# Kernel optimization log

Hardware: AMD Instinct MI355X
Metric: run time of the kernel (lower is better)

The kernel has to match this reference:

```python
import jax, jax.numpy as jnp
import numpy as np

G, VPG, CPG, LPC = 32, 512, 1024, 3
N_VARS, N_CLAUSES = G * VPG, G * CPG
N_LITS = N_CLAUSES * LPC
FM, QM, ROUNDS = 128, 32, 4
EPS_NORM, EPS_LOG, EPS_SQRT = 1e-6, 1e-8, 1e-6


def _dense_init(key, fin, fout):
    w = jax.random.normal(key, (fin, fout), jnp.float32) * np.float32(np.sqrt(2.0 / (fin + fout)))
    return w, jnp.zeros((fout,), jnp.float32)


def setup_inputs():
    rng = np.random.default_rng(0)
    g_of_clause = np.repeat(np.arange(G), CPG)
    lit_clause = np.repeat(np.arange(N_CLAUSES), LPC).astype(np.int32)
    # each clause picks LPC variables from its own graph's variable block
    lit_var = (np.repeat(g_of_clause * VPG, LPC) + rng.integers(0, VPG, N_LITS)).astype(np.int32)
    lit_sign = (rng.integers(0, 2, N_LITS) * 2 - 1).astype(np.int32)  # +/-1 literal polarity
    variables_mask = np.repeat(np.arange(G), VPG).astype(np.int32)
    clauses_mask = g_of_clause.astype(np.int32)
    keys = jax.random.split(jax.random.key(0), 13)
    inp = dict(
        lit_var=jnp.asarray(lit_var), lit_sign=jnp.asarray(lit_sign), lit_clause=jnp.asarray(lit_clause),
        variables_mask=jnp.asarray(variables_mask), clauses_mask=jnp.asarray(clauses_mask),
        noise=jax.random.normal(keys[12], (ROUNDS, N_VARS, 4), jnp.float32),
    )
    dims = dict(vq=(FM + 4, 2 * QM, QM), cm=(FM + QM, 3 * FM, FM + QM), ug=(FM + 3 * QM, 2 * FM, FM), vo=(FM, FM, 1))
    ki = 0
    for name, (fin, hid, fout) in dims.items():
        for i, (a, b) in enumerate([(fin, hid), (hid, hid), (hid, fout)]):
            w, bb = _dense_init(keys[ki], a, b); ki += 1
            inp[f'{name}_w{i}'] = w
            inp[f'{name}_b{i}'] = bb
    return inp


def _mlp(x, ps):
    # repo MLP: (layer_count-1) hidden Dense with leaky_relu(0.2), linear output, no layer norm
    for w, b in ps[:-1]:
        x = jax.nn.leaky_relu(x @ w + b, negative_slope=0.2)
    w, b = ps[-1]
    return x @ w + b


def _zero_state(n, f):
    # one_hot(0) - 1/f, scaled by sqrt(f)*0.25
    oh = jnp.zeros((n, f), jnp.float32).at[:, 0].set(1.0)
    return (oh - 1.0 / f) * np.float32(np.sqrt(f) * 0.25)


def _forward(lit_var, lit_sign, lit_clause, variables_mask, clauses_mask, noise, params, checkpoint=False):
    p = list(params)
    vq = [(p[0], p[1]), (p[2], p[3]), (p[4], p[5])]
    cm = [(p[6], p[7]), (p[8], p[9]), (p[10], p[11])]
    ug = [(p[12], p[13]), (p[14], p[15]), (p[16], p[17])]
    vo = [(p[18], p[19]), (p[20], p[21]), (p[22], p[23])]
    seg_sum = jax.ops.segment_sum
    sgn = lit_sign.astype(jnp.float32)[:, None]          # [L,1] +/-1
    pos = (sgn > 0).astype(jnp.float32)
    neg = 1.0 - pos
    var_cnt = seg_sum(jnp.ones((N_VARS,), jnp.float32), variables_mask, G)
    cls_cnt = seg_sum(jnp.ones((N_CLAUSES,), jnp.float32), clauses_mask, G)

    def pair_norm(x, seg, cnt):
        mean = seg_sum(x, seg, G) / cnt[:, None]
        x = x - mean[seg]
        return x * jax.lax.rsqrt(jnp.mean(jnp.square(x), axis=-1, keepdims=True) + EPS_NORM)

    def clause_val(q):
        # softplus_loss: V_c = exp(-sum_{lit in c} softplus(sign * q[var]))  -> [N_CLAUSES, d]
        lit = jax.nn.softplus(q[lit_var] * sgn)
        return jnp.exp(-seg_sum(lit, lit_clause, N_CLAUSES))

    def body(carry, noise_t):
        variables, clause_state = carry
        v1 = jnp.concatenate([variables, noise_t], axis=-1)          # [V, FM+4]
        query = _mlp(v1, vq)                                          # [V, QM]

        def q_loss(q):
            cl = clause_val(q)
            return jnp.sum(cl), cl
        variables_grad, clauses_loss = jax.grad(q_loss, has_aux=True)(query)

        clause_data = _mlp(jnp.concatenate([clause_state, clauses_loss], axis=-1), cm)  # [C, FM+QM]
        vloss = clause_data[:, :QM]
        new_cv = pair_norm(clause_data[:, QM:], clauses_mask, cls_cnt) * 0.25
        clause_state = new_cv + 0.1 * clause_state

        contrib = vloss[lit_clause]                                   # [L, QM]
        loss_pos = seg_sum(contrib * pos, lit_var, N_VARS)            # A_pos @ vloss
        loss_neg = seg_sum(contrib * neg, lit_var, N_VARS)            # A_neg @ vloss

        unit = jnp.concatenate([variables, variables_grad, loss_pos, loss_neg], axis=-1)
        new_vars = pair_norm(_mlp(unit, ug), variables_mask, var_cnt) * 0.25
        variables = new_vars + 0.1 * variables

        logits = _mlp(variables, vo)                                  # [V, 1]
        v = clause_val(logits)
        per_clause = v * (-jnp.log(1.0 - v + EPS_LOG))                # softplus_mixed_loss
        per_graph = seg_sum(per_clause, clauses_mask, G)              # [G, 1]
        logit_loss = jnp.sum(jnp.sqrt(per_graph + EPS_SQRT))

        variables = jax.lax.stop_gradient(variables) * 0.2 + variables * 0.8
        clause_state = jax.lax.stop_gradient(clause_state) * 0.2 + clause_state * 0.8
        return (variables, clause_state), (logit_loss, logits)

    if checkpoint:
        body = jax.checkpoint(body)
    init = (_zero_state(N_VARS, FM), _zero_state(N_CLAUSES, FM))
    _, (step_losses, logits_seq) = jax.lax.scan(body, init, noise)
    return logits_seq[-1], jnp.sum(step_losses) / np.float32(ROUNDS)


def reference(lit_var, lit_sign, lit_clause, variables_mask, clauses_mask, noise,
              vq_w0, vq_b0, vq_w1, vq_b1, vq_w2, vq_b2,
              cm_w0, cm_b0, cm_w1, cm_b1, cm_w2, cm_b2,
              ug_w0, ug_b0, ug_w1, ug_b1, ug_w2, ug_b2,
              vo_w0, vo_b0, vo_w1, vo_b1, vo_w2, vo_b2):
    params = (vq_w0, vq_b0, vq_w1, vq_b1, vq_w2, vq_b2,
              cm_w0, cm_b0, cm_w1, cm_b1, cm_w2, cm_b2,
              ug_w0, ug_b0, ug_w1, ug_b1, ug_w2, ug_b2,
              vo_w0, vo_b0, vo_w1, vo_b1, vo_w2, vo_b2)
    return _forward(lit_var, lit_sign, lit_clause, variables_mask, clauses_mask, noise, params)
```

## Files before the change

### kernel.cpp

```cpp
#include <hip/hip_runtime.h>
#include <hip/hip_bf16.h>
#include <math.h>

#define NG     32
#define NVARS  16384
#define NCLS   32768
#define NLITS  98304
#define NROUNDS 4

typedef __attribute__((ext_vector_type(8))) short bf16x8;
typedef __attribute__((ext_vector_type(4))) float f32x4;

#define OFF_VAR    ((size_t)0)
#define OFF_CST    ((size_t)2097152)
#define OFF_XCMB   ((size_t)6291456)
#define OFF_XUGB   ((size_t)9437184)
#define OFF_ABUF   ((size_t)11534336)
#define OFF_BBUF   ((size_t)17825792)
#define OFF_CD     ((size_t)24117248)
#define OFF_Q      ((size_t)30408704)
#define OFF_CLF    ((size_t)30932992)
#define OFF_VLOSS  ((size_t)31981568)
#define OFF_CMEAN  ((size_t)33030144)
#define OFF_VMEAN  ((size_t)33034240)
#define OFF_LOSS   ((size_t)33038336)
#define OFF_CSO    ((size_t)33038340)
#define OFF_CSE    ((size_t)33054725)
#define OFF_CSC    ((size_t)33153029)
#define OFF_WT     ((size_t)33169416)

#define WT_CM0  ((size_t)0)
#define WT_CM1  ((size_t)73728)
#define WT_CM2  ((size_t)221184)
#define WT_UG0  ((size_t)294912)
#define WT_UG1  ((size_t)360448)
#define WT_UG2  ((size_t)425984)
#define WT_VO0  ((size_t)458752)
#define WT_VO1  ((size_t)475136)
#define WT_VQ0  ((size_t)491520)
#define WT_VQ1  ((size_t)501760)
#define WT_VQ2  ((size_t)505856)

__device__ __forceinline__ float softplus_f(float x) {
  return fmaxf(x, 0.f) + log1pf(expf(-fabsf(x)));
}
__device__ __forceinline__ short f2bf(float x) {
  __hip_bfloat16 h = __float2bfloat16(x);
  return *reinterpret_cast<short*>(&h);
}
__device__ __forceinline__ float bf2f(short s) {
  __hip_bfloat16 h = *reinterpret_cast<__hip_bfloat16*>(&s);
  return __bfloat162float(h);
}

__global__ void init_state_kernel(float* __restrict__ var, float* __restrict__ cst,
                                  short* __restrict__ xugb, short* __restrict__ xcmb,
                                  float* __restrict__ loss, int* __restrict__ cnt) {
  int t = blockIdx.x * blockDim.x + threadIdx.x;
  if (t == 0) *loss = 0.f;
  const int main_total = (NVARS + NCLS) * 128;
  if (t < main_total) {
    int row = t >> 7, m = t & 127;
    const float base = 2.82842712474619f;
    float val = ((m == 0) ? (1.f - 1.f / 128.f) : (-1.f / 128.f)) * base;
    if (row < NVARS) {
      var[(size_t)row * 128 + m] = val;
      xugb[(size_t)row * 256 + m] = f2bf(val);
    } else {
      int c = row - NVARS;
      cst[(size_t)c * 128 + m] = val;
      xcmb[(size_t)c * 192 + m] = f2bf(val);
    }
    return;
  }
  int t2 = t - main_total;
  if (t2 < NVARS * 32) {
    int row = t2 >> 5, j = t2 & 31;
    xugb[(size_t)row * 256 + 224 + j] = 0;
    return;
  }
  int t3 = t2 - NVARS * 32;
  if (t3 < NCLS * 32) {
    int row = t3 >> 5, j = t3 & 31;
    xcmb[(size_t)row * 192 + 160 + j] = 0;
    return;
  }
  int t4 = t3 - NCLS * 32;
  if (t4 < NVARS) cnt[t4] = 0;
}

__global__ void csr_count_kernel(const int* __restrict__ lit_var, int* __restrict__ cnt) {
  int l = blockIdx.x * blockDim.x + threadIdx.x;
  if (l >= NLITS) return;
  atomicAdd(&cnt[lit_var[l]], 1);
}

__global__ __launch_bounds__(1024) void csr_scan_kernel(const int* __restrict__ cnt,
                                                        int* __restrict__ cso,
                                                        int* __restrict__ cur) {
  __shared__ int part[1024];
  int t = threadIdx.x;
  int base = t * 16;
  int local[16];
  int s = 0;
  #pragma unroll
  for (int i = 0; i < 16; ++i) { local[i] = cnt[base + i]; s += local[i]; }
  part[t] = s;
  __syncthreads();
  for (int off = 1; off < 1024; off <<= 1) {
    int v = (t >= off) ? part[t - off] : 0;
    __syncthreads();
    part[t] += v;
    __syncthreads();
  }
  int run = part[t] - s;
  #pragma unroll
  for (int i = 0; i < 16; ++i) {
    cso[base + i] = run;
    cur[base + i] = run;
    run += local[i];
  }
  if (t == 1023) cso[NVARS] = run;
}

__global__ void csr_fill_kernel(const int* __restrict__ lit_var, const int* __restrict__ lit_sign,
                                const int* __restrict__ lit_clause,
                                int* __restrict__ cur, int* __restrict__ cse) {
  int l = blockIdx.x * blockDim.x + threadIdx.x;
  if (l >= NLITS) return;
  int v = lit_var[l];
  int pos = atomicAdd(&cur[v], 1);
  cse[pos] = (lit_clause[l] << 1) | (lit_sign[l] > 0 ? 1 : 0);
}

__global__ void convert_all_kernel(
    const float* __restrict__ cm_w0, const float* __restrict__ cm_w1, const float* __restrict__ cm_w2,
    const float* __restrict__ ug_w0, const float* __restrict__ ug_w1, const float* __restrict__ ug_w2,
    const float* __restrict__ vo_w0, const float* __restrict__ vo_w1,
    const float* __restrict__ vq_w0, const float* __restrict__ vq_w1, const float* __restrict__ vq_w2,
    short* __restrict__ wt) {
  int t = blockIdx.x * blockDim.x + threadIdx.x;
  const float* W; int K, N, Kp; size_t base; int idx;
  if      (t < 73728)  { W = cm_w0; K = 160; N = 384; Kp = 192; base = WT_CM0; idx = t; }
  else if (t < 221184) { W = cm_w1; K = 384; N = 384; Kp = 384; base = WT_CM1; idx = t - 73728; }
  else if (t < 294912) { W = cm_w2; K = 384; N = 160; Kp = 384; base = WT_CM2; idx = t - 221184; }
  else if (t < 360448) { W = ug_w0; K = 224; N = 256; Kp = 256; base = WT_UG0; idx = t - 294912; }
  else if (t < 425984) { W = ug_w1; K = 256; N = 256; Kp = 256; base = WT_UG1; idx = t - 360448; }
  else if (t < 458752) { W = ug_w2; K = 256; N = 128; Kp = 256; base = WT_UG2; idx = t - 425984; }
  else if (t < 475136) { W = vo_w0; K = 128; N = 128; Kp = 128; base = WT_VO0; idx = t - 458752; }
  else if (t < 491520) { W = vo_w1; K = 128; N = 128; Kp = 128; base = WT_VO1; idx = t - 475136; }
  else if (t < 501760) { W = vq_w0; K = 132; N = 64;  Kp = 160; base = WT_VQ0; idx = t - 491520; }
  else if (t < 505856) { W = vq_w1; K = 64;  N = 64;  Kp = 64;  base = WT_VQ1; idx = t - 501760; }
  else if (t < 507904) { W = vq_w2; K = 64;  N = 32;  Kp = 64;  base = WT_VQ2; idx = t - 505856; }
  else return;
  int n = idx / Kp, k = idx - n * Kp;
  float v = (k < K && n < N) ? W[(size_t)k * N + n] : 0.f;
  wt[base + idx] = f2bf(v);
}

__global__ __launch_bounds__(256) void fused_vq_kernel(
    const short* __restrict__ xugb, const float* __restrict__ noise,
    const short* __restrict__ w0, const short* __restrict__ w1, const short* __restrict__ w2,
    const float* __restrict__ b0, const float* __restrict__ b1, const float* __restrict__ b2,
    float* __restrict__ Q) {
  __shared__ short A[64 * 160];
  __shared__ short H1[4][16 * 64];
  __shared__ short H2[4][16 * 64];
  const int wid = threadIdx.x >> 6, lane = threadIdx.x & 63;
  const int rbase = blockIdx.x * 64 + wid * 16;
  #pragma unroll
  for (int i = 0; i < 4; ++i) {
    int s = i * 64 + lane;
    int row = s >> 4, c8 = s & 15;
    *(bf16x8*)&A[(wid * 16 + row) * 160 + c8 * 8] =
        *(const bf16x8*)&xugb[(size_t)(rbase + row) * 256 + c8 * 8];
  }
  {
    int row = lane >> 2, seg = lane & 3;
    bf16x8 z = {0, 0, 0, 0, 0, 0, 0, 0};
    if (seg == 0) {
      float4 nz = *(const float4*)&noise[(size_t)(rbase + row) * 4];
      z[0] = f2bf(nz.x); z[1] = f2bf(nz.y); z[2] = f2bf(nz.z); z[3] = f2bf(nz.w);
    }
    *(bf16x8*)&A[(wid * 16 + row) * 160 + 128 + seg * 8] = z;
  }
  const int kof = (lane >> 4) * 8;
  const int l15 = lane & 15;
  f32x4 acc[4] = {};
  #pragma unroll
  for (int ks = 0; ks < 5; ++ks) {
    bf16x8 a = *(const bf16x8*)&A[(wid * 16 + l15) * 160 + ks * 32 + kof];
    #pragma unroll
    for (int ni = 0; ni < 4; ++ni) {
      bf16x8 b = *(const bf16x8*)&w0[(ni * 16 + l15) * 160 + ks * 32 + kof];
      acc[ni] = __builtin_amdgcn_mfma_f32_16x16x32_bf16(a, b, acc[ni], 0, 0, 0);
    }
  }
  #pragma unroll
  for (int ni = 0; ni < 4; ++ni) {
    int col = ni * 16 + l15;
    float bb = b0[col];
    #pragma unroll
    for (int j = 0; j < 4; ++j) {
      float v = acc[ni][j] + bb; v = v > 0.f ? v : 0.2f * v;
      H1[wid][((lane >> 4) * 4 + j) * 64 + col] = f2bf(v);
    }
  }
  f32x4 acc2[4] = {};
  #pragma unroll
  for (int ks = 0; ks < 2; ++ks) {
    bf16x8 a = *(const bf16x8*)&H1[wid][l15 * 64 + ks * 32 + kof];
    #pragma unroll
    for (int ni = 0; ni < 4; ++ni) {
      bf16x8 b = *(const bf16x8*)&w1[(ni * 16 + l15) * 64 + ks * 32 + kof];
      acc2[ni] = __builtin_amdgcn_mfma_f32_16x16x32_bf16(a, b, acc2[ni], 0, 0, 0);
    }
  }
  #pragma unroll
  for (int ni = 0; ni < 4; ++ni) {
    int col = ni * 16 + l15;
    float bb = b1[col];
    #pragma unroll
    for (int j = 0; j < 4; ++j) {
      float v = acc2[ni][j] + bb; v = v > 0.f ? v : 0.2f * v;
      H2[wid][((lane >> 4) * 4 + j) * 64 + col] = f2bf(v);
    }
  }
  f32x4 acc3[2] = {};
  #pragma unroll
  for (int ks = 0; ks < 2; ++ks) {
    bf16x8 a = *(const bf16x8*)&H2[wid][l15 * 64 + ks * 32 + kof];
    #pragma unroll
    for (int ni = 0; ni < 2; ++ni) {
      bf16x8 b = *(const bf16x8*)&w2[(ni * 16 + l15) * 64 + ks * 32 + kof];
      acc3[ni] = __builtin_amdgcn_mfma_f32_16x16x32_bf16(a, b, acc3[ni], 0, 0, 0);
    }
  }
  #pragma unroll
  for (int ni = 0; ni < 2; ++ni) {
    int col = ni * 16 + l15;
    float bb = b2[col];
    #pragma unroll
    for (int j = 0; j < 4; ++j)
      Q[(size_t)(rbase + (lane >> 4) * 4 + j) * 32 + col] = acc3[ni][j] + bb;
  }
}

__global__ void fused_clause_kernel(const float* __restrict__ Q, const int* __restrict__ lit_var,
                                    const int* __restrict__ lit_sign,
                                    short* __restrict__ xcmb, float* __restrict__ clf,
                                    float* __restrict__ meanz) {
  int t = blockIdx.x * blockDim.x + threadIdx.x;
  if (t < 2 * 32 * 128) meanz[t] = 0.f;
  if (t >= NCLS * 32) return;
  int c = t >> 5, m = t & 31;
  int l0 = 3 * c;
  int v0 = lit_var[l0], v1 = lit_var[l0 + 1], v2 = lit_var[l0 + 2];
  int s0 = lit_sign[l0], s1 = lit_sign[l0 + 1], s2 = lit_sign[l0 + 2];
  float q0 = Q[(size_t)v0 * 32 + m];
  float q1 = Q[(size_t)v1 * 32 + m];
  float q2 = Q[(size_t)v2 * 32 + m];
  float sp = softplus_f(q0 * (float)s0) + softplus_f(q1 * (float)s1) + softplus_f(q2 * (float)s2);
  float cl = expf(-sp);
  clf[(size_t)c * 32 + m] = cl;
  xcmb[(size_t)c * 192 + 128 + m] = f2bf(cl);
}

template<int TN, bool RELU, bool OUTBF16, int EPI>
__global__ __launch_bounds__(256) void gemm_mfma_kernel(
    const short* __restrict__ A, int lda,
    const short* __restrict__ Wt,
    const float* __restrict__ bias, int nbias,
    void* __restrict__ Cout, int Np, int Kp,
    float* __restrict__ aux,
    float* __restrict__ meanbuf, float inv_cnt, int gshift) {
  constexpr int NB = TN / 32;
  __shared__ short As[128 * 64];
  __shared__ short Bs[TN * 64];
  const int bn = blockIdx.x * TN;
  const int bm = blockIdx.y * 128;
  const int tid  = threadIdx.x;
  const int wid  = tid >> 6;
  const int lane = tid & 63;
  const int wm = (wid >> 1) * 64;
  const int wn = (wid & 1) * (TN / 2);

  f32x4 acc[4][NB] = {};

  for (int k0 = 0; k0 < Kp; k0 += 64) {
    #pragma unroll
    for (int i = 0; i < 4; ++i) {
      int s = (i * 4 + wid) * 64 + lane;
      int row = s >> 3, cs = (s & 7) << 3;
      const short* src = A + (size_t)(bm + row) * lda + k0 + cs;
      __builtin_amdgcn_global_load_lds(
          (const __attribute__((address_space(1))) void*)src,
          (__attribute__((address_space(3))) void*)(As + (size_t)(i * 4 + wid) * 64 * 8),
          16, 0, 0);
    }
    #pragma unroll
    for (int i = 0; i < TN / 32; ++i) {
      int s = (i * 4 + wid) * 64 + lane;
      int n = s >> 3, cs = (s & 7) << 3;
      const short* src = Wt + (size_t)(bn + n) * Kp + k0 + cs;
      __builtin_amdgcn_global_load_lds(
          (const __attribute__((address_space(1))) void*)src,
          (__attribute__((address_space(3))) void*)(Bs + (size_t)(i * 4 + wid) * 64 * 8),
          16, 0, 0);
    }
    __syncthreads();

    #pragma unroll
    for (int ks = 0; ks < 2; ++ks) {
      const int kof = ks * 32 + (lane >> 4) * 8;
      bf16x8 a[4], b[NB];
      #pragma unroll
      for (int mi = 0; mi < 4; ++mi)
        a[mi] = *(const bf16x8*)&As[(wm + mi * 16 + (lane & 15)) * 64 + kof];
      #pragma unroll
      for (int ni = 0; ni < NB; ++ni)
        b[ni] = *(const bf16x8*)&Bs[(wn + ni * 16 + (lane & 15)) * 64 + kof];
      #pragma unroll
      for (int mi = 0; mi < 4; ++mi)
        #pragma unroll
        for (int ni = 0; ni < NB; ++ni)
          acc[mi][ni] = __builtin_amdgcn_mfma_f32_16x16x32_bf16(a[mi], b[ni], acc[mi][ni], 0, 0, 0);
    }
    __syncthreads();
  }

  const int col0 = bn + wn + (lane & 15);
  const int row0 = bm + wm + (lane >> 4) * 4;
  #pragma unroll
  for (int ni = 0; ni < NB; ++ni) {
    int col = col0 + ni * 16;
    float bv = (col < nbias) ? bias[col] : 0.f;
    float colsum = 0.f;
    #pragma unroll
    for (int mi = 0; mi < 4; ++mi) {
      #pragma unroll
      for (int j = 0; j < 4; ++j) {
        int row = row0 + mi * 16 + j;
        float v = acc[mi][ni][j] + bv;
        if (EPI == 0) {
          if (RELU) v = v > 0.f ? v : 0.2f * v;
          if (OUTBF16) ((short*)Cout)[(size_t)row * Np + col] = f2bf(v);
          else         ((float*)Cout)[(size_t)row * Np + col] = v;
        } else if (EPI == 1) {
          if (col < 32) {
            aux[(size_t)row * 32 + col] = v;
          } else if (col < 160) {
            ((float*)Cout)[(size_t)row * Np + col] = v;
            colsum += v;
          }
        } else {
          ((float*)Cout)[(size_t)row * Np + col] = v;
          colsum += v;
        }
      }
    }
    if ((EPI == 1 && col >= 32 && col < 160) || EPI == 2) {
      colsum += __shfl_xor(colsum, 16);
      colsum += __shfl_xor(colsum, 32);
      if ((lane >> 4) == 0) {
        int midx = (EPI == 1) ? (col - 32) : col;
        atomicAdd(&meanbuf[(size_t)(bm >> gshift) * 128 + midx], colsum * inv_cnt);
      }
    }
  }
}

__global__ __launch_bounds__(256) void pnc_gather_kernel(
    const float* __restrict__ CD, const float* __restrict__ cmean,
    float* __restrict__ cst, short* __restrict__ xcmb,
    const float* __restrict__ Q, const int* __restrict__ cso, const int* __restrict__ cse,
    const float* __restrict__ clf, const float* __restrict__ vloss,
    short* __restrict__ xugb) {
  int b = blockIdx.x;
  if (b < NCLS / 4) {
    int wid = threadIdx.x >> 6;
    int lane = threadIdx.x & 63;
    int row = b * 4 + wid;
    int g = row >> 10;
    const float* xp = CD + (size_t)row * 192 + 32;
    float y0 = xp[lane]      - cmean[g * 128 + lane];
    float y1 = xp[lane + 64] - cmean[g * 128 + lane + 64];
    float ss = y0 * y0 + y1 * y1;
    #pragma unroll
    for (int o = 32; o > 0; o >>= 1) ss += __shfl_xor(ss, o);
    float inv = rsqrtf(ss * (1.f / 128.f) + 1e-6f);
    float* sp = cst + (size_t)row * 128;
    float s0 = y0 * inv * 0.25f + 0.1f * sp[lane];
    float s1 = y1 * inv * 0.25f + 0.1f * sp[lane + 64];
    sp[lane]      = s0;
    sp[lane + 64] = s1;
    xcmb[(size_t)row * 192 + lane]      = f2bf(s0);
    xcmb[(size_t)row * 192 + lane + 64] = f2bf(s1);
  } else {
    int t = (b - NCLS / 4) * 256 + threadIdx.x;
    int v = t >> 5, m = t & 31;
    float q = Q[(size_t)v * 32 + m];
    float sig = 1.f / (1.f + expf(-q));
    float vgs = 0.f, lps = 0.f, lns = 0.f;
    int e0 = cso[v], e1 = cso[v + 1];
    for (int e = e0; e < e1; ++e) {
      int ent = cse[e];
      int c = ent >> 1;
      bool pos = ent & 1;
      float clc = clf[(size_t)c * 32 + m];
      vgs -= clc * (sig - (pos ? 0.f : 1.f));
      float vl = vloss[(size_t)c * 32 + m];
      if (pos) lps += vl; else lns += vl;
    }
    short* xp = xugb + (size_t)v * 256 + 128;
    xp[m]      = f2bf(vgs);
    xp[32 + m] = f2bf(lps);
    xp[64 + m] = f2bf(lns);
  }
}

__global__ __launch_bounds__(256) void pairnorm_update_kernel(
    const float* __restrict__ x, int stride, int coloff,
    const float* __restrict__ mean, float* __restrict__ state,
    short* __restrict__ bout, int bstride, int rows_per_g) {
  int wid = threadIdx.x >> 6;
  int lane = threadIdx.x & 63;
  int row = blockIdx.x * 4 + wid;
  int g = row / rows_per_g;
  const float* xp = x + (size_t)row * stride + coloff;
  float y0 = xp[lane]      - mean[g * 128 + lane];
  float y1 = xp[lane + 64] - mean[g * 128 + lane + 64];
  float ss = y0 * y0 + y1 * y1;
  #pragma unroll
  for (int o = 32; o > 0; o >>= 1) ss += __shfl_xor(ss, o);
  float inv = rsqrtf(ss * (1.f / 128.f) + 1e-6f);
  float* sp = state + (size_t)row * 128;
  float s0 = y0 * inv * 0.25f + 0.1f * sp[lane];
  float s1 = y1 * inv * 0.25f + 0.1f * sp[lane + 64];
  sp[lane]      = s0;
  sp[lane + 64] = s1;
  bout[(size_t)row * bstride + lane]      = f2bf(s0);
  bout[(size_t)row * bstride + lane + 64] = f2bf(s1);
}

__global__ __launch_bounds__(256) void fused_vo_kernel(
    const short* __restrict__ xugb,
    const short* __restrict__ w0, const short* __restrict__ w1,
    const float* __restrict__ b0, const float* __restrict__ b1,
    const float* __restrict__ w2, const float* __restrict__ b2,
    float* __restrict__ logits) {
  __shared__ short A[64 * 128];
  __shared__ short H1[4][16 * 128];
  __shared__ short H2[4][16 * 128];
  const int wid = threadIdx.x >> 6, lane = threadIdx.x & 63;
  const int rbase = blockIdx.x * 64 + wid * 16;
  #pragma unroll
  for (int i = 0; i < 4; ++i) {
    int s = i * 64 + lane;
    int row = s >> 4, c8 = s & 15;
    *(bf16x8*)&A[(wid * 16 + row) * 128 + c8 * 8] =
        *(const bf16x8*)&xugb[(size_t)(rbase + row) * 256 + c8 * 8];
  }
  const int kof = (lane >> 4) * 8;
  const int l15 = lane & 15;
  f32x4 acc[8] = {};
  #pragma unroll
  for (int ks = 0; ks < 4; ++ks) {
    bf16x8 a = *(const bf16x8*)&A[(wid * 16 + l15) * 128 + ks * 32 + kof];
    #pragma unroll
    for (int ni = 0; ni < 8; ++ni) {
      bf16x8 b = *(const bf16x8*)&w0[(ni * 16 + l15) * 128 + ks * 32 + kof];
      acc[ni] = __builtin_amdgcn_mfma_f32_16x16x32_bf16(a, b, acc[ni], 0, 0, 0);
    }
  }
  #pragma unroll
  for (int ni = 0; ni < 8; ++ni) {
    int col = ni * 16 + l15;
    float bb = b0[col];
    #pragma unroll
    for (int j = 0; j < 4; ++j) {
      float v = acc[ni][j] + bb; v = v > 0.f ? v : 0.2f * v;
      H1[wid][((lane >> 4) * 4 + j) * 128 + col] = f2bf(v);
    }
  }
  f32x4 acc2[8] = {};
  #pragma unroll
  for (int ks = 0; ks < 4; ++ks) {
    bf16x8 a = *(const bf16x8*)&H1[wid][l15 * 128 + ks * 32 + kof];
    #pragma unroll
    for (int ni = 0; ni < 8; ++ni) {
      bf16x8 b = *(const bf16x8*)&w1[(ni * 16 + l15) * 128 + ks * 32 + kof];
      acc2[ni] = __builtin_amdgcn_mfma_f32_16x16x32_bf16(a, b, acc2[ni], 0, 0, 0);
    }
  }
  #pragma unroll
  for (int ni = 0; ni < 8; ++ni) {
    int col = ni * 16 + l15;
    float bb = b1[col];
    #pragma unroll
    for (int j = 0; j < 4; ++j) {
      float v = acc2[ni][j] + bb; v = v > 0.f ? v : 0.2f * v;
      H2[wid][((lane >> 4) * 4 + j) * 128 + col] = f2bf(v);
    }
  }
  {
    int row = lane >> 2, q = lane & 3;
    float s = 0.f;
    #pragma unroll
    for (int jj = 0; jj < 4; ++jj) {
      bf16x8 h = *(const bf16x8*)&H2[wid][row * 128 + q * 32 + jj * 8];
      #pragma unroll
      for (int e = 0; e < 8; ++e) s += bf2f(h[e]) * w2[q * 32 + jj * 8 + e];
    }
    s += __shfl_xor(s, 1);
    s += __shfl_xor(s, 2);
    if (q == 0) logits[rbase + row] = s + b2[0];
  }
}

__global__ __launch_bounds__(1024) void fused_loss_kernel(
    const float* __restrict__ logits, const int* __restrict__ lit_var,
    const int* __restrict__ lit_sign, float* __restrict__ loss) {
  __shared__ float lg[512];
  __shared__ float red[16];
  int g = blockIdx.x, tid = threadIdx.x;
  if (tid < 512) lg[tid] = logits[(size_t)g * 512 + tid];
  __syncthreads();
  int c = g * 1024 + tid;
  float s = 0.f;
  #pragma unroll
  for (int i = 0; i < 3; ++i) {
    int l = 3 * c + i;
    float sg = (float)lit_sign[l];
    s += softplus_f(lg[lit_var[l] - g * 512] * sg);
  }
  float vv = expf(-s);
  float pcv = vv * (-logf(1.f - vv + 1e-8f));
  #pragma unroll
  for (int o = 32; o > 0; o >>= 1) pcv += __shfl_xor(pcv, o);
  if ((tid & 63) == 0) red[tid >> 6] = pcv;
  __syncthreads();
  if (tid < 16) {
    float x = red[tid];
    #pragma unroll
    for (int o = 8; o > 0; o >>= 1) x += __shfl_xor(x, o);
    if (tid == 0) atomicAdd(loss, sqrtf(x + 1e-6f));
  }
}

__global__ void finalize_kernel(const float* __restrict__ loss_acc, float* __restrict__ out) {
  out[0] = loss_acc[0] * 0.25f;
}

extern "C" void kernel_launch(void* const* d_in, const int* in_sizes, int n_in,
                              void* d_out, int out_size, void* d_ws, size_t ws_size,
                              hipStream_t stream) {
  const int* lit_var    = (const int*)d_in[0];
  const int* lit_sign   = (const int*)d_in[1];
  const int* lit_clause = (const int*)d_in[2];
  const float* noise    = (const float*)d_in[5];
  const float* vq_w0 = (const float*)d_in[6];   const float* vq_b0 = (const float*)d_in[7];
  const float* vq_w1 = (const float*)d_in[8];   const float* vq_b1 = (const float*)d_in[9];
  const float* vq_w2 = (const float*)d_in[10];  const float* vq_b2 = (const float*)d_in[11];
  const float* cm_w0 = (const float*)d_in[12];  const float* cm_b0 = (const float*)d_in[13];
  const float* cm_w1 = (const float*)d_in[14];  const float* cm_b1 = (const float*)d_in[15];
  const float* cm_w2 = (const float*)d_in[16];  const float* cm_b2 = (const float*)d_in[17];
  const float* ug_w0 = (const float*)d_in[18];  const float* ug_b0 = (const float*)d_in[19];
  const float* ug_w1 = (const float*)d_in[20];  const float* ug_b1 = (const float*)d_in[21];
  const float* ug_w2 = (const float*)d_in[22];  const float* ug_b2 = (const float*)d_in[23];
  const float* vo_w0 = (const float*)d_in[24];  const float* vo_b0 = (const float*)d_in[25];
  const float* vo_w1 = (const float*)d_in[26];  const float* vo_b1 = (const float*)d_in[27];
  const float* vo_w2 = (const float*)d_in[28];  const float* vo_b2 = (const float*)d_in[29];

  float* ws = (float*)d_ws;
  float* var   = ws + OFF_VAR;
  float* cst   = ws + OFF_CST;
  short* xcmb  = (short*)(ws + OFF_XCMB);
  short* xugb  = (short*)(ws + OFF_XUGB);
  short* bufA  = (short*)(ws + OFF_ABUF);
  short* bufB  = (short*)(ws + OFF_BBUF);
  float* CD    = ws + OFF_CD;
  float* Q     = ws + OFF_Q;
  float* clf   = ws + OFF_CLF;
  float* vloss = ws + OFF_VLOSS;
  float* cmean = ws + OFF_CMEAN;
  float* vmean = ws + OFF_VMEAN;
  float* loss  = ws + OFF_LOSS;
  int*   cso   = (int*)(ws + OFF_CSO);
  int*   cse   = (int*)(ws + OFF_CSE);
  int*   csc   = (int*)(ws + OFF_CSC);
  short* wt    = (short*)(ws + OFF_WT);
  float* logits = (float*)d_out;
  float* loss_out = (float*)d_out + NVARS;

  convert_all_kernel<<<1984, 256, 0, stream>>>(cm_w0, cm_w1, cm_w2, ug_w0, ug_w1, ug_w2,
                                               vo_w0, vo_w1, vq_w0, vq_w1, vq_w2, wt);
  init_state_kernel<<<30784, 256, 0, stream>>>(var, cst, xugb, xcmb, loss, csc);
  csr_count_kernel<<<NLITS / 256, 256, 0, stream>>>(lit_var, csc);
  csr_scan_kernel<<<1, 1024, 0, stream>>>(csc, cso, csc);
  csr_fill_kernel<<<NLITS / 256, 256, 0, stream>>>(lit_var, lit_sign, lit_clause, csc, cse);

  for (int r = 0; r < NROUNDS; ++r) {
    const float* noise_r = noise + (size_t)r * NVARS * 4;

    fused_vq_kernel<<<NVARS / 64, 256, 0, stream>>>(
        xugb, noise_r, wt + WT_VQ0, wt + WT_VQ1, wt + WT_VQ2, vq_b0, vq_b1, vq_b2, Q);

    fused_clause_kernel<<<NCLS * 32 / 256, 256, 0, stream>>>(Q, lit_var, lit_sign, xcmb, clf, cmean);

    gemm_mfma_kernel<128, true, true, 0><<<dim3(3, NCLS / 128), 256, 0, stream>>>(
        xcmb, 192, wt + WT_CM0, cm_b0, 384, bufA, 384, 192, nullptr, nullptr, 0.f, 0);
    gemm_mfma_kernel<128, true, true, 0><<<dim3(3, NCLS / 128), 256, 0, stream>>>(
        bufA, 384, wt + WT_CM1, cm_b1, 384, bufB, 384, 384, nullptr, nullptr, 0.f, 0);
    gemm_mfma_kernel<64, false, false, 1><<<dim3(3, NCLS / 128), 256, 0, stream>>>(
        bufB, 384, wt + WT_CM2, cm_b2, 160, CD, 192, 384, vloss, cmean, 1.f / 1024.f, 10);

    pnc_gather_kernel<<<NCLS / 4 + NVARS * 32 / 256, 256, 0, stream>>>(
        CD, cmean, cst, xcmb, Q, cso, cse, clf, vloss, xugb);

    gemm_mfma_kernel<128, true, true, 0><<<dim3(2, NVARS / 128), 256, 0, stream>>>(
        xugb, 256, wt + WT_UG0, ug_b0, 256, bufA, 256, 256, nullptr, nullptr, 0.f, 0);
    gemm_mfma_kernel<128, true, true, 0><<<dim3(2, NVARS / 128), 256, 0, stream>>>(
        bufA, 256, wt + WT_UG1, ug_b1, 256, bufB, 256, 256, nullptr, nullptr, 0.f, 0);
    gemm_mfma_kernel<64, false, false, 2><<<dim3(2, NVARS / 128), 256, 0, stream>>>(
        bufB, 256, wt + WT_UG2, ug_b2, 128, CD, 128, 256, nullptr, vmean, 1.f / 512.f, 9);

    pairnorm_update_kernel<<<NVARS / 4, 256, 0, stream>>>(CD, 128, 0, vmean, var, xugb, 256, 512);

    fused_vo_kernel<<<NVARS / 64, 256, 0, stream>>>(
        xugb, wt + WT_VO0, wt + WT_VO1, vo_b0, vo_b1, vo_w2, vo_b2, logits);

    fused_loss_kernel<<<NG, 1024, 0, stream>>>(logits, lit_var, lit_sign, loss);
  }

  finalize_kernel<<<1, 1, 0, stream>>>(loss, loss_out);
}
```

Before: 682.1 us.

## Fuse clause gather into UG0 GEMM, pairnorm into VO, loss into VQ

Per-variable CSR gather now runs inside a new UG0 GEMM kernel that builds the gathered K-slices straight in LDS, and the clause pairnorm runs in extra blocks of the same launch. Variable pairnorm moves into the VO kernel prologue. The per-round loss moves into the next round's VQ kernel, with one final loss launch after the loop. The goal is to drop three launches per round and the global round-trips of intermediate tensors, at the cost of serialising the gather inside GEMM blocks (only 256 GEMM blocks do the gather work) and losing the LDS-cached logits in the loss.

After: 931.5 us. 36.6% more time.

```diff
diff --git a/kernel.cpp b/kernel.cpp
--- a/kernel.cpp
+++ b/kernel.cpp
@@ -73,13 +73,7 @@
     }
     return;
   }
-  int t2 = t - main_total;
-  if (t2 < NVARS * 32) {
-    int row = t2 >> 5, j = t2 & 31;
-    xugb[(size_t)row * 256 + 224 + j] = 0;
-    return;
-  }
-  int t3 = t2 - NVARS * 32;
+  int t3 = t - main_total;
   if (t3 < NCLS * 32) {
     int row = t3 >> 5, j = t3 & 31;
     xcmb[(size_t)row * 192 + 160 + j] = 0;
@@ -162,11 +156,38 @@
     const short* __restrict__ xugb, const float* __restrict__ noise,
     const short* __restrict__ w0, const short* __restrict__ w1, const short* __restrict__ w2,
     const float* __restrict__ b0, const float* __restrict__ b1, const float* __restrict__ b2,
-    float* __restrict__ Q) {
+    float* __restrict__ Q,
+    const float* __restrict__ logits_in, const int* __restrict__ lit_var,
+    const int* __restrict__ lit_sign, float* __restrict__ loss, int do_loss) {
   __shared__ short A[64 * 160];
   __shared__ short H1[4][16 * 64];
   __shared__ short H2[4][16 * 64];
+  __shared__ float lred[4];
   const int wid = threadIdx.x >> 6, lane = threadIdx.x & 63;
+  if (do_loss && blockIdx.x < NG) {
+    int g = blockIdx.x;
+    float part = 0.f;
+    #pragma unroll
+    for (int k = 0; k < 4; ++k) {
+      int c = g * 1024 + k * 256 + threadIdx.x;
+      int l0 = 3 * c;
+      float s = 0.f;
+      #pragma unroll
+      for (int i = 0; i < 3; ++i) {
+        int l = l0 + i;
+        float sg = (float)lit_sign[l];
+        s += softplus_f(logits_in[lit_var[l]] * sg);
+      }
+      float vv = expf(-s);
+      part += vv * (-logf(1.f - vv + 1e-8f));
+    }
+    #pragma unroll
+    for (int o = 32; o > 0; o >>= 1) part += __shfl_xor(part, o);
+    if (lane == 0) lred[wid] = part;
+    __syncthreads();
+    if (threadIdx.x == 0)
+      atomicAdd(loss, sqrtf(lred[0] + lred[1] + lred[2] + lred[3] + 1e-6f));
+  }
   const int rbase = blockIdx.x * 64 + wid * 16;
   #pragma unroll
   for (int i = 0; i < 4; ++i) {
@@ -370,81 +391,145 @@
   }
 }
 
-__global__ __launch_bounds__(256) void pnc_gather_kernel(
-    const float* __restrict__ CD, const float* __restrict__ cmean,
-    float* __restrict__ cst, short* __restrict__ xcmb,
+__global__ __launch_bounds__(256) void ug0_pnc_kernel(
+    const short* __restrict__ xugb, const short* __restrict__ Wt,
+    const float* __restrict__ bias, short* __restrict__ Cout,
     const float* __restrict__ Q, const int* __restrict__ cso, const int* __restrict__ cse,
     const float* __restrict__ clf, const float* __restrict__ vloss,
-    short* __restrict__ xugb) {
-  int b = blockIdx.x;
-  if (b < NCLS / 4) {
-    int wid = threadIdx.x >> 6;
-    int lane = threadIdx.x & 63;
-    int row = b * 4 + wid;
-    int g = row >> 10;
-    const float* xp = CD + (size_t)row * 192 + 32;
-    float y0 = xp[lane]      - cmean[g * 128 + lane];
-    float y1 = xp[lane + 64] - cmean[g * 128 + lane + 64];
-    float ss = y0 * y0 + y1 * y1;
-    #pragma unroll
-    for (int o = 32; o > 0; o >>= 1) ss += __shfl_xor(ss, o);
-    float inv = rsqrtf(ss * (1.f / 128.f) + 1e-6f);
-    float* sp = cst + (size_t)row * 128;
-    float s0 = y0 * inv * 0.25f + 0.1f * sp[lane];
-    float s1 = y1 * inv * 0.25f + 0.1f * sp[lane + 64];
-    sp[lane]      = s0;
-    sp[lane + 64] = s1;
-    xcmb[(size_t)row * 192 + lane]      = f2bf(s0);
-    xcmb[(size_t)row * 192 + lane + 64] = f2bf(s1);
-  } else {
-    int t = (b - NCLS / 4) * 256 + threadIdx.x;
-    int v = t >> 5, m = t & 31;
-    float q = Q[(size_t)v * 32 + m];
-    float sig = 1.f / (1.f + expf(-q));
-    float vgs = 0.f, lps = 0.f, lns = 0.f;
-    int e0 = cso[v], e1 = cso[v + 1];
-    for (int e = e0; e < e1; ++e) {
-      int ent = cse[e];
-      int c = ent >> 1;
-      bool pos = ent & 1;
-      float clc = clf[(size_t)c * 32 + m];
-      vgs -= clc * (sig - (pos ? 0.f : 1.f));
-      float vl = vloss[(size_t)c * 32 + m];
-      if (pos) lps += vl; else lns += vl;
-    }
-    short* xp = xugb + (size_t)v * 256 + 128;
-    xp[m]      = f2bf(vgs);
-    xp[32 + m] = f2bf(lps);
-    xp[64 + m] = f2bf(lns);
-  }
-}
-
-__global__ __launch_bounds__(256) void pairnorm_update_kernel(
-    const float* __restrict__ x, int stride, int coloff,
-    const float* __restrict__ mean, float* __restrict__ state,
-    short* __restrict__ bout, int bstride, int rows_per_g) {
-  int wid = threadIdx.x >> 6;
-  int lane = threadIdx.x & 63;
-  int row = blockIdx.x * 4 + wid;
-  int g = row / rows_per_g;
-  const float* xp = x + (size_t)row * stride + coloff;
-  float y0 = xp[lane]      - mean[g * 128 + lane];
-  float y1 = xp[lane + 64] - mean[g * 128 + lane + 64];
-  float ss = y0 * y0 + y1 * y1;
-  #pragma unroll
-  for (int o = 32; o > 0; o >>= 1) ss += __shfl_xor(ss, o);
-  float inv = rsqrtf(ss * (1.f / 128.f) + 1e-6f);
-  float* sp = state + (size_t)row * 128;
-  float s0 = y0 * inv * 0.25f + 0.1f * sp[lane];
-  float s1 = y1 * inv * 0.25f + 0.1f * sp[lane + 64];
-  sp[lane]      = s0;
-  sp[lane + 64] = s1;
-  bout[(size_t)row * bstride + lane]      = f2bf(s0);
-  bout[(size_t)row * bstride + lane + 64] = f2bf(s1);
+    const float* __restrict__ CD, const float* __restrict__ cmean,
+    float* __restrict__ cst, short* __restrict__ xcmb) {
+  __shared__ short As[128 * 64];
+  __shared__ short Bs[128 * 64];
+  __shared__ short side[128 * 32];
+  const int bid = blockIdx.x;
+  const int tid = threadIdx.x;
+  const int wid = tid >> 6, lane = tid & 63;
+
+  if (bid >= 256) {
+    int pb = bid - 256;
+    #pragma unroll
+    for (int rr = 0; rr < 4; ++rr) {
+      int row = pb * 16 + wid * 4 + rr;
+      int g = row >> 10;
+      const float* xp = CD + (size_t)row * 192 + 32;
+      float y0 = xp[lane]      - cmean[g * 128 + lane];
+      float y1 = xp[lane + 64] - cmean[g * 128 + 64 + lane];
+      float ss = y0 * y0 + y1 * y1;
+      #pragma unroll
+      for (int o = 32; o > 0; o >>= 1) ss += __shfl_xor(ss, o);
+      float inv = rsqrtf(ss * (1.f / 128.f) + 1e-6f);
+      float* sp = cst + (size_t)row * 128;
+      float s0 = y0 * inv * 0.25f + 0.1f * sp[lane];
+      float s1 = y1 * inv * 0.25f + 0.1f * sp[lane + 64];
+      sp[lane]      = s0;
+      sp[lane + 64] = s1;
+      xcmb[(size_t)row * 192 + lane]      = f2bf(s0);
+      xcmb[(size_t)row * 192 + 64 + lane] = f2bf(s1);
+    }
+    return;
+  }
+
+  const int bn = (bid & 1) * 128;
+  const int bm = (bid >> 1) * 128;
+  const int wm = (wid >> 1) * 64;
+  const int wn = (wid & 1) * 64;
+  f32x4 acc[4][4] = {};
+
+  for (int k0 = 0; k0 < 256; k0 += 64) {
+    #pragma unroll
+    for (int i = 0; i < 4; ++i) {
+      int s = (i * 4 + wid) * 64 + lane;
+      int n = s >> 3, cs = (s & 7) << 3;
+      const short* src = Wt + (size_t)(bn + n) * 256 + k0 + cs;
+      __builtin_amdgcn_global_load_lds(
+          (const __attribute__((address_space(1))) void*)src,
+          (__attribute__((address_space(3))) void*)(Bs + (size_t)(i * 4 + wid) * 64 * 8),
+          16, 0, 0);
+    }
+    if (k0 < 128) {
+      #pragma unroll
+      for (int i = 0; i < 4; ++i) {
+        int s = (i * 4 + wid) * 64 + lane;
+        int row = s >> 3, cs = (s & 7) << 3;
+        const short* src = xugb + (size_t)(bm + row) * 256 + k0 + cs;
+        __builtin_amdgcn_global_load_lds(
+            (const __attribute__((address_space(1))) void*)src,
+            (__attribute__((address_space(3))) void*)(As + (size_t)(i * 4 + wid) * 64 * 8),
+            16, 0, 0);
+      }
+    } else if (k0 == 128) {
+      int m = tid & 31, set = tid >> 5;
+      for (int i = 0; i < 16; ++i) {
+        int lrow = set * 16 + i;
+        int v = bm + lrow;
+        float q = Q[(size_t)v * 32 + m];
+        float sig = 1.f / (1.f + expf(-q));
+        float vgs = 0.f, lps = 0.f, lns = 0.f;
+        int e0 = cso[v], e1 = cso[v + 1];
+        for (int e = e0; e < e1; ++e) {
+          int ent = cse[e];
+          int c = ent >> 1;
+          bool pos = ent & 1;
+          float clc = clf[(size_t)c * 32 + m];
+          vgs -= clc * (sig - (pos ? 0.f : 1.f));
+          float vl = vloss[(size_t)c * 32 + m];
+          if (pos) lps += vl; else lns += vl;
+        }
+        As[lrow * 64 + m]      = f2bf(vgs);
+        As[lrow * 64 + 32 + m] = f2bf(lps);
+        side[lrow * 32 + m]    = f2bf(lns);
+      }
+    } else {
+      int m = tid & 31, set = tid >> 5;
+      for (int i = 0; i < 16; ++i) {
+        int lrow = set * 16 + i;
+        As[lrow * 64 + m]      = side[lrow * 32 + m];
+        As[lrow * 64 + 32 + m] = 0;
+      }
+    }
+    __syncthreads();
+
+    #pragma unroll
+    for (int ks = 0; ks < 2; ++ks) {
+      const int kof = ks * 32 + (lane >> 4) * 8;
+      bf16x8 a[4], b[4];
+      #pragma unroll
+      for (int mi = 0; mi < 4; ++mi)
+        a[mi] = *(const bf16x8*)&As[(wm + mi * 16 + (lane & 15)) * 64 + kof];
+      #pragma unroll
+      for (int ni = 0; ni < 4; ++ni)
+        b[ni] = *(const bf16x8*)&Bs[(wn + ni * 16 + (lane & 15)) * 64 + kof];
+      #pragma unroll
+      for (int mi = 0; mi < 4; ++mi)
+        #pragma unroll
+        for (int ni = 0; ni < 4; ++ni)
+          acc[mi][ni] = __builtin_amdgcn_mfma_f32_16x16x32_bf16(a[mi], b[ni], acc[mi][ni], 0, 0, 0);
+    }
+    __syncthreads();
+  }
+
+  const int col0 = bn + wn + (lane & 15);
+  const int row0 = bm + wm + (lane >> 4) * 4;
+  #pragma unroll
+  for (int ni = 0; ni < 4; ++ni) {
+    int col = col0 + ni * 16;
+    float bv = bias[col];
+    #pragma unroll
+    for (int mi = 0; mi < 4; ++mi) {
+      #pragma unroll
+      for (int j = 0; j < 4; ++j) {
+        int row = row0 + mi * 16 + j;
+        float v = acc[mi][ni][j] + bv;
+        v = v > 0.f ? v : 0.2f * v;
+        Cout[(size_t)row * 256 + col] = f2bf(v);
+      }
+    }
+  }
 }
 
 __global__ __launch_bounds__(256) void fused_vo_kernel(
-    const short* __restrict__ xugb,
+    const float* __restrict__ CD, const float* __restrict__ vmean,
+    float* __restrict__ var, short* __restrict__ xugb,
     const short* __restrict__ w0, const short* __restrict__ w1,
     const float* __restrict__ b0, const float* __restrict__ b1,
     const float* __restrict__ w2, const float* __restrict__ b2,
@@ -454,12 +539,24 @@
   __shared__ short H2[4][16 * 128];
   const int wid = threadIdx.x >> 6, lane = threadIdx.x & 63;
   const int rbase = blockIdx.x * 64 + wid * 16;
-  #pragma unroll
-  for (int i = 0; i < 4; ++i) {
-    int s = i * 64 + lane;
-    int row = s >> 4, c8 = s & 15;
-    *(bf16x8*)&A[(wid * 16 + row) * 128 + c8 * 8] =
-        *(const bf16x8*)&xugb[(size_t)(rbase + row) * 256 + c8 * 8];
+  for (int i = 0; i < 16; ++i) {
+    int row = rbase + i;
+    int g = row >> 9;
+    float y0 = CD[(size_t)row * 128 + lane]      - vmean[g * 128 + lane];
+    float y1 = CD[(size_t)row * 128 + 64 + lane] - vmean[g * 128 + 64 + lane];
+    float ss = y0 * y0 + y1 * y1;
+    #pragma unroll
+    for (int o = 32; o > 0; o >>= 1) ss += __shfl_xor(ss, o);
+    float inv = rsqrtf(ss * (1.f / 128.f) + 1e-6f);
+    float* vp = var + (size_t)row * 128;
+    float s0 = y0 * inv * 0.25f + 0.1f * vp[lane];
+    float s1 = y1 * inv * 0.25f + 0.1f * vp[lane + 64];
+    vp[lane]      = s0;
+    vp[lane + 64] = s1;
+    xugb[(size_t)row * 256 + lane]      = f2bf(s0);
+    xugb[(size_t)row * 256 + 64 + lane] = f2bf(s1);
+    A[(wid * 16 + i) * 128 + lane]      = f2bf(s0);
+    A[(wid * 16 + i) * 128 + 64 + lane] = f2bf(s1);
   }
   const int kof = (lane >> 4) * 8;
   const int l15 = lane & 15;
@@ -521,18 +618,15 @@
 __global__ __launch_bounds__(1024) void fused_loss_kernel(
     const float* __restrict__ logits, const int* __restrict__ lit_var,
     const int* __restrict__ lit_sign, float* __restrict__ loss) {
-  __shared__ float lg[512];
   __shared__ float red[16];
   int g = blockIdx.x, tid = threadIdx.x;
-  if (tid < 512) lg[tid] = logits[(size_t)g * 512 + tid];
-  __syncthreads();
   int c = g * 1024 + tid;
   float s = 0.f;
   #pragma unroll
   for (int i = 0; i < 3; ++i) {
     int l = 3 * c + i;
     float sg = (float)lit_sign[l];
-    s += softplus_f(lg[lit_var[l] - g * 512] * sg);
+    s += softplus_f(logits[lit_var[l]] * sg);
   }
   float vv = expf(-s);
   float pcv = vv * (-logf(1.f - vv + 1e-8f));
@@ -595,7 +689,7 @@
 
   convert_all_kernel<<<1984, 256, 0, stream>>>(cm_w0, cm_w1, cm_w2, ug_w0, ug_w1, ug_w2,
                                                vo_w0, vo_w1, vq_w0, vq_w1, vq_w2, wt);
-  init_state_kernel<<<30784, 256, 0, stream>>>(var, cst, xugb, xcmb, loss, csc);
+  init_state_kernel<<<28736, 256, 0, stream>>>(var, cst, xugb, xcmb, loss, csc);
   csr_count_kernel<<<NLITS / 256, 256, 0, stream>>>(lit_var, csc);
   csr_scan_kernel<<<1, 1024, 0, stream>>>(csc, cso, csc);
   csr_fill_kernel<<<NLITS / 256, 256, 0, stream>>>(lit_var, lit_sign, lit_clause, csc, cse);
@@ -604,7 +698,8 @@
     const float* noise_r = noise + (size_t)r * NVARS * 4;
 
     fused_vq_kernel<<<NVARS / 64, 256, 0, stream>>>(
-        xugb, noise_r, wt + WT_VQ0, wt + WT_VQ1, wt + WT_VQ2, vq_b0, vq_b1, vq_b2, Q);
+        xugb, noise_r, wt + WT_VQ0, wt + WT_VQ1, wt + WT_VQ2, vq_b0, vq_b1, vq_b2, Q,
+        logits, lit_var, lit_sign, loss, r > 0 ? 1 : 0);
 
     fused_clause_kernel<<<NCLS * 32 / 256, 256, 0, stream>>>(Q, lit_var, lit_sign, xcmb, clf, cmean);
 
@@ -615,23 +710,18 @@
     gemm_mfma_kernel<64, false, false, 1><<<dim3(3, NCLS / 128), 256, 0, stream>>>(
         bufB, 384, wt + WT_CM2, cm_b2, 160, CD, 192, 384, vloss, cmean, 1.f / 1024.f, 10);
 
-    pnc_gather_kernel<<<NCLS / 4 + NVARS * 32 / 256, 256, 0, stream>>>(
-        CD, cmean, cst, xcmb, Q, cso, cse, clf, vloss, xugb);
-
-    gemm_mfma_kernel<128, true, true, 0><<<dim3(2, NVARS / 128), 256, 0, stream>>>(
-        xugb, 256, wt + WT_UG0, ug_b0, 256, bufA, 256, 256, nullptr, nullptr, 0.f, 0);
+    ug0_pnc_kernel<<<256 + 2048, 256, 0, stream>>>(
+        xugb, wt + WT_UG0, ug_b0, bufA, Q, cso, cse, clf, vloss, CD, cmean, cst, xcmb);
+
     gemm_mfma_kernel<128, true, true, 0><<<dim3(2, NVARS / 128), 256, 0, stream>>>(
         bufA, 256, wt + WT_UG1, ug_b1, 256, bufB, 256, 256, nullptr, nullptr, 0.f, 0);
     gemm_mfma_kernel<64, false, false, 2><<<dim3(2, NVARS / 128), 256, 0, stream>>>(
         bufB, 256, wt + WT_UG2, ug_b2, 128, CD, 128, 256, nullptr, vmean, 1.f / 512.f, 9);
 
-    pairnorm_update_kernel<<<NVARS / 4, 256, 0, stream>>>(CD, 128, 0, vmean, var, xugb, 256, 512);
-
     fused_vo_kernel<<<NVARS / 64, 256, 0, stream>>>(
-        xugb, wt + WT_VO0, wt + WT_VO1, vo_b0, vo_b1, vo_w2, vo_b2, logits);
-
-    fused_loss_kernel<<<NG, 1024, 0, stream>>>(logits, lit_var, lit_sign, loss);
-  }
-
+        CD, vmean, var, xugb, wt + WT_VO0, wt + WT_VO1, vo_b0, vo_b1, vo_w2, vo_b2, logits);
+  }
+
+  fused_loss_kernel<<<NG, 1024, 0, stream>>>(logits, lit_var, lit_sign, loss);
   finalize_kernel<<<1, 1, 0, stream>>>(loss, loss_out);
 }
```

## Fuse pairnorm update into VO kernel and loss into next round's VQ

Applied to the files above, without the earlier changes.

Removes the standalone pairnorm_update kernel by computing the variable pairnorm and state update inside fused_vo_kernel while staging its A tile. The per-round loss kernel is folded into the first 32 blocks of the next round's fused_vq_kernel, and only the final round's loss runs as a separate launch after the loop. This cuts two kernel launches per round and one round trip of the bf16 state through global memory. In exchange, the pairnorm rows are processed serially per wave, and the first 32 VQ blocks carry extra loss work and a block-wide sync.

After: 716.8 us. +5.1%, slower.

```diff
diff --git a/kernel.cpp b/kernel.cpp
--- a/kernel.cpp
+++ b/kernel.cpp
@@ -162,11 +162,38 @@
     const short* __restrict__ xugb, const float* __restrict__ noise,
     const short* __restrict__ w0, const short* __restrict__ w1, const short* __restrict__ w2,
     const float* __restrict__ b0, const float* __restrict__ b1, const float* __restrict__ b2,
-    float* __restrict__ Q) {
+    float* __restrict__ Q,
+    const float* __restrict__ logits_in, const int* __restrict__ lit_var,
+    const int* __restrict__ lit_sign, float* __restrict__ loss, int do_loss) {
   __shared__ short A[64 * 160];
   __shared__ short H1[4][16 * 64];
   __shared__ short H2[4][16 * 64];
+  __shared__ float lred[4];
   const int wid = threadIdx.x >> 6, lane = threadIdx.x & 63;
+  if (do_loss && blockIdx.x < NG) {
+    int g = blockIdx.x;
+    float part = 0.f;
+    #pragma unroll
+    for (int k = 0; k < 4; ++k) {
+      int c = g * 1024 + k * 256 + threadIdx.x;
+      int l0 = 3 * c;
+      float s = 0.f;
+      #pragma unroll
+      for (int i = 0; i < 3; ++i) {
+        int l = l0 + i;
+        float sg = (float)lit_sign[l];
+        s += softplus_f(logits_in[lit_var[l]] * sg);
+      }
+      float vv = expf(-s);
+      part += vv * (-logf(1.f - vv + 1e-8f));
+    }
+    #pragma unroll
+    for (int o = 32; o > 0; o >>= 1) part += __shfl_xor(part, o);
+    if (lane == 0) lred[wid] = part;
+    __syncthreads();
+    if (threadIdx.x == 0)
+      atomicAdd(loss, sqrtf(lred[0] + lred[1] + lred[2] + lred[3] + 1e-6f));
+  }
   const int rbase = blockIdx.x * 64 + wid * 16;
   #pragma unroll
   for (int i = 0; i < 4; ++i) {
@@ -419,32 +446,9 @@
   }
 }
 
-__global__ __launch_bounds__(256) void pairnorm_update_kernel(
-    const float* __restrict__ x, int stride, int coloff,
-    const float* __restrict__ mean, float* __restrict__ state,
-    short* __restrict__ bout, int bstride, int rows_per_g) {
-  int wid = threadIdx.x >> 6;
-  int lane = threadIdx.x & 63;
-  int row = blockIdx.x * 4 + wid;
-  int g = row / rows_per_g;
-  const float* xp = x + (size_t)row * stride + coloff;
-  float y0 = xp[lane]      - mean[g * 128 + lane];
-  float y1 = xp[lane + 64] - mean[g * 128 + lane + 64];
-  float ss = y0 * y0 + y1 * y1;
-  #pragma unroll
-  for (int o = 32; o > 0; o >>= 1) ss += __shfl_xor(ss, o);
-  float inv = rsqrtf(ss * (1.f / 128.f) + 1e-6f);
-  float* sp = state + (size_t)row * 128;
-  float s0 = y0 * inv * 0.25f + 0.1f * sp[lane];
-  float s1 = y1 * inv * 0.25f + 0.1f * sp[lane + 64];
-  sp[lane]      = s0;
-  sp[lane + 64] = s1;
-  bout[(size_t)row * bstride + lane]      = f2bf(s0);
-  bout[(size_t)row * bstride + lane + 64] = f2bf(s1);
-}
-
 __global__ __launch_bounds__(256) void fused_vo_kernel(
-    const short* __restrict__ xugb,
+    const float* __restrict__ CD, const float* __restrict__ vmean,
+    float* __restrict__ var, short* __restrict__ xugb,
     const short* __restrict__ w0, const short* __restrict__ w1,
     const float* __restrict__ b0, const float* __restrict__ b1,
     const float* __restrict__ w2, const float* __restrict__ b2,
@@ -454,12 +458,24 @@
   __shared__ short H2[4][16 * 128];
   const int wid = threadIdx.x >> 6, lane = threadIdx.x & 63;
   const int rbase = blockIdx.x * 64 + wid * 16;
-  #pragma unroll
-  for (int i = 0; i < 4; ++i) {
-    int s = i * 64 + lane;
-    int row = s >> 4, c8 = s & 15;
-    *(bf16x8*)&A[(wid * 16 + row) * 128 + c8 * 8] =
-        *(const bf16x8*)&xugb[(size_t)(rbase + row) * 256 + c8 * 8];
+  for (int i = 0; i < 16; ++i) {
+    int row = rbase + i;
+    int g = row >> 9;
+    float y0 = CD[(size_t)row * 128 + lane]      - vmean[g * 128 + lane];
+    float y1 = CD[(size_t)row * 128 + 64 + lane] - vmean[g * 128 + 64 + lane];
+    float ss = y0 * y0 + y1 * y1;
+    #pragma unroll
+    for (int o = 32; o > 0; o >>= 1) ss += __shfl_xor(ss, o);
+    float inv = rsqrtf(ss * (1.f / 128.f) + 1e-6f);
+    float* vp = var + (size_t)row * 128;
+    float s0 = y0 * inv * 0.25f + 0.1f * vp[lane];
+    float s1 = y1 * inv * 0.25f + 0.1f * vp[lane + 64];
+    vp[lane]      = s0;
+    vp[lane + 64] = s1;
+    xugb[(size_t)row * 256 + lane]      = f2bf(s0);
+    xugb[(size_t)row * 256 + 64 + lane] = f2bf(s1);
+    A[(wid * 16 + i) * 128 + lane]      = f2bf(s0);
+    A[(wid * 16 + i) * 128 + 64 + lane] = f2bf(s1);
   }
   const int kof = (lane >> 4) * 8;
   const int l15 = lane & 15;
@@ -521,18 +537,15 @@
 __global__ __launch_bounds__(1024) void fused_loss_kernel(
     const float* __restrict__ logits, const int* __restrict__ lit_var,
     const int* __restrict__ lit_sign, float* __restrict__ loss) {
-  __shared__ float lg[512];
   __shared__ float red[16];
   int g = blockIdx.x, tid = threadIdx.x;
-  if (tid < 512) lg[tid] = logits[(size_t)g * 512 + tid];
-  __syncthreads();
   int c = g * 1024 + tid;
   float s = 0.f;
   #pragma unroll
   for (int i = 0; i < 3; ++i) {
     int l = 3 * c + i;
     float sg = (float)lit_sign[l];
-    s += softplus_f(lg[lit_var[l] - g * 512] * sg);
+    s += softplus_f(logits[lit_var[l]] * sg);
   }
   float vv = expf(-s);
   float pcv = vv * (-logf(1.f - vv + 1e-8f));
@@ -604,7 +617,8 @@
     const float* noise_r = noise + (size_t)r * NVARS * 4;
 
     fused_vq_kernel<<<NVARS / 64, 256, 0, stream>>>(
-        xugb, noise_r, wt + WT_VQ0, wt + WT_VQ1, wt + WT_VQ2, vq_b0, vq_b1, vq_b2, Q);
+        xugb, noise_r, wt + WT_VQ0, wt + WT_VQ1, wt + WT_VQ2, vq_b0, vq_b1, vq_b2, Q,
+        logits, lit_var, lit_sign, loss, r > 0 ? 1 : 0);
 
     fused_clause_kernel<<<NCLS * 32 / 256, 256, 0, stream>>>(Q, lit_var, lit_sign, xcmb, clf, cmean);
 
@@ -625,13 +639,10 @@
     gemm_mfma_kernel<64, false, false, 2><<<dim3(2, NVARS / 128), 256, 0, stream>>>(
         bufB, 256, wt + WT_UG2, ug_b2, 128, CD, 128, 256, nullptr, vmean, 1.f / 512.f, 9);
 
-    pairnorm_update_kernel<<<NVARS / 4, 256, 0, stream>>>(CD, 128, 0, vmean, var, xugb, 256, 512);
-
     fused_vo_kernel<<<NVARS / 64, 256, 0, stream>>>(
-        xugb, wt + WT_VO0, wt + WT_VO1, vo_b0, vo_b1, vo_w2, vo_b2, logits);
-
-    fused_loss_kernel<<<NG, 1024, 0, stream>>>(logits, lit_var, lit_sign, loss);
-  }
-
+        CD, vmean, var, xugb, wt + WT_VO0, wt + WT_VO1, vo_b0, vo_b1, vo_w2, vo_b2, logits);
+  }
+
+  fused_loss_kernel<<<NG, 1024, 0, stream>>>(logits, lit_var, lit_sign, loss);
   finalize_kernel<<<1, 1, 0, stream>>>(loss, loss_out);
 }
```
